# Optimization experiments

Hardware: AMD Instinct MI355X
Metric: run time of the kernel (lower is better)

Reference implementation:

```python
import jax, jax.numpy as jnp
import numpy as np
from jax import lax

VOCAB, MAX_LEN, EMB, H = 50000, 128, 300, 50
BATCH = 1024
BN_SCALE = 1.0 / np.sqrt(1.0 + 0.001)  # batch_normalization with mean=0, var=1, eps=1e-3


def setup_inputs() -> dict:
    key = jax.random.key(0)
    ks = jax.random.split(key, 10)
    return {
        "x1": jax.random.randint(ks[0], (BATCH, MAX_LEN), 0, VOCAB, dtype=jnp.int32),
        "x2": jax.random.randint(ks[1], (BATCH, MAX_LEN), 0, VOCAB, dtype=jnp.int32),
        "embedding_matrix": jax.random.normal(ks[2], (VOCAB, EMB), jnp.float32),
        "W_fw": jax.random.normal(ks[3], (EMB + H, 4 * H), jnp.float32) * 0.05,
        "b_fw": jnp.zeros((4 * H,), jnp.float32),
        "W_bw": jax.random.normal(ks[4], (EMB + H, 4 * H), jnp.float32) * 0.05,
        "b_bw": jnp.zeros((4 * H,), jnp.float32),
        "W1": jax.random.normal(ks[5], (2 * H, 25), jnp.float32) * 0.1,
        "b1": jax.random.normal(ks[6], (25,), jnp.float32) * 0.1,
        "W2": jax.random.normal(ks[7], (25, 3), jnp.float32) * 0.1,
        "b2": jax.random.normal(ks[8], (3,), jnp.float32) * 0.1,
    }


def _lstm_scan(xs, W, b):
    # xs: [T, B, E]; BasicLSTMCell: gates = [x, h] @ W + b, split i, j, f, o; forget_bias=1.0
    T, B, _ = xs.shape
    def step(carry, x):
        c, h = carry
        g = jnp.concatenate([x, h], axis=-1) @ W + b
        i, j, f, o = jnp.split(g, 4, axis=-1)
        c2 = c * jax.nn.sigmoid(f + 1.0) + jax.nn.sigmoid(i) * jnp.tanh(j)
        h2 = jnp.tanh(c2) * jax.nn.sigmoid(o)
        return (c2, h2), h2
    init = (jnp.zeros((B, H), xs.dtype), jnp.zeros((B, H), xs.dtype))
    _, hs = lax.scan(step, init, xs)
    return hs  # [T, B, H]


def reference(x1, x2, embedding_matrix, W_fw, b_fw, W_bw, b_bw, W1, b1, W2, b2):
    tokens = jnp.concatenate([x1, x2], axis=1)            # [B, 2*max_len]
    emb = embedding_matrix[tokens]                         # [B, T, E]
    xs = jnp.transpose(emb, (1, 0, 2))                     # [T, B, E]
    h_fw = _lstm_scan(xs, W_fw, b_fw)                      # [T, B, H]
    h_bw = _lstm_scan(xs[::-1], W_bw, b_bw)                # [T, B, H] (time reversed)
    # static_bidirectional_rnn reverses bw outputs, so outputs[-1] pairs
    # fw at step T-1 with bw's first step (which consumed x_{T-1}).
    feat = jnp.concatenate([h_fw[-1], h_bw[0]], axis=-1)   # [B, 2H]
    bn = feat * BN_SCALE
    h1 = jax.nn.relu(bn @ W1 + b1)                         # dropout omitted (eval mode)
    out = h1 @ W2 + b2
    return out * BN_SCALE
```

## Files before the change

### kernel.cpp

```cpp
#include <hip/hip_runtime.h>
#include <hip/hip_bf16.h>


#define VOCAB 50000
#define EMB   300
#define HID   50
#define GATES 200
#define BATCH 1024
#define TT    256
#define NPAD  208
#define KPAD  320
#define BN_SCALE 0.9995003746877732f

typedef short bf16x8 __attribute__((ext_vector_type(8)));
typedef float f32x4  __attribute__((ext_vector_type(4)));

__device__ __forceinline__ float sigm(float x) {
    return 1.0f / (1.0f + __expf(-x));
}
__device__ __forceinline__ float tanh_f(float x) {
    return 1.0f - 2.0f / (__expf(2.0f * x) + 1.0f);
}
__device__ __forceinline__ unsigned short f32_to_bf16(float x) {
    unsigned int u = __float_as_uint(x);
    u += 0x7fffu + ((u >> 16) & 1u);
    return (unsigned short)(u >> 16);
}
__device__ __forceinline__ float bf16_to_f32(unsigned short h) {
    return __uint_as_float(((unsigned int)h) << 16);
}

__global__ __launch_bounds__(256) void split_w(const float* __restrict__ Wfw,
                                               unsigned short* __restrict__ WhT,
                                               unsigned short* __restrict__ WlT) {
    const int idx = blockIdx.x * 256 + threadIdx.x;
    if (idx >= NPAD * KPAD) return;
    const int n = idx / KPAD;
    const int k = idx - n * KPAD;
    float v = (n < GATES && k < EMB) ? Wfw[k * GATES + n] : 0.0f;
    const unsigned short hb = f32_to_bf16(v);
    const unsigned short lb = f32_to_bf16(v - bf16_to_f32(hb));
    WhT[idx] = hb;
    WlT[idx] = lb;
}

__global__ __launch_bounds__(256, 1) void vocab_proj_mfma(const float* __restrict__ E,
                                                          const unsigned short* __restrict__ WhT,
                                                          const unsigned short* __restrict__ WlT,
                                                          float* __restrict__ P) {
    const int w  = threadIdx.x >> 6;
    const int l  = threadIdx.x & 63;
    const int lr = l & 15;
    const int lg = l >> 4;

    const int row0 = blockIdx.x * 128 + w * 32 + lr;
    const int row1 = row0 + 16;
    const int rc0  = (row0 < VOCAB) ? row0 : (VOCAB - 1);
    const int rc1  = (row1 < VOCAB) ? row1 : (VOCAB - 1);
    const float* Erow0 = E + (size_t)rc0 * EMB;
    const float* Erow1 = E + (size_t)rc1 * EMB;

    f32x4 acc0[13], acc1[13];
#pragma unroll
    for (int f = 0; f < 13; ++f) {
        acc0[f] = (f32x4){0.f, 0.f, 0.f, 0.f};
        acc1[f] = (f32x4){0.f, 0.f, 0.f, 0.f};
    }

    for (int ks = 0; ks < 10; ++ks) {
        const int k0 = ks * 32 + lg * 8;
        float av0[8], av1[8];
        if (ks < 9) {
            const float4 a00 = *reinterpret_cast<const float4*>(Erow0 + k0);
            const float4 a01 = *reinterpret_cast<const float4*>(Erow0 + k0 + 4);
            const float4 a10 = *reinterpret_cast<const float4*>(Erow1 + k0);
            const float4 a11 = *reinterpret_cast<const float4*>(Erow1 + k0 + 4);
            av0[0]=a00.x; av0[1]=a00.y; av0[2]=a00.z; av0[3]=a00.w;
            av0[4]=a01.x; av0[5]=a01.y; av0[6]=a01.z; av0[7]=a01.w;
            av1[0]=a10.x; av1[1]=a10.y; av1[2]=a10.z; av1[3]=a10.w;
            av1[4]=a11.x; av1[5]=a11.y; av1[6]=a11.z; av1[7]=a11.w;
        } else {
#pragma unroll
            for (int j = 0; j < 8; ++j) {
                const int kk = k0 + j;
                av0[j] = (kk < EMB) ? Erow0[kk] : 0.0f;
                av1[j] = (kk < EMB) ? Erow1[kk] : 0.0f;
            }
        }
        bf16x8 ah0, al0, ah1, al1;
#pragma unroll
        for (int j = 0; j < 8; ++j) {
            unsigned short hb = f32_to_bf16(av0[j]);
            ah0[j] = (short)hb;
            al0[j] = (short)f32_to_bf16(av0[j] - bf16_to_f32(hb));
            hb = f32_to_bf16(av1[j]);
            ah1[j] = (short)hb;
            al1[j] = (short)f32_to_bf16(av1[j] - bf16_to_f32(hb));
        }

#pragma unroll
        for (int f = 0; f < 13; ++f) {
            const int n = f * 16 + lr;
            const size_t boff = (size_t)n * KPAD + k0;
            const bf16x8 bh = *reinterpret_cast<const bf16x8*>(WhT + boff);
            const bf16x8 bl = *reinterpret_cast<const bf16x8*>(WlT + boff);
            acc0[f] = __builtin_amdgcn_mfma_f32_16x16x32_bf16(ah0, bh, acc0[f], 0, 0, 0);
            acc0[f] = __builtin_amdgcn_mfma_f32_16x16x32_bf16(al0, bh, acc0[f], 0, 0, 0);
            acc0[f] = __builtin_amdgcn_mfma_f32_16x16x32_bf16(ah0, bl, acc0[f], 0, 0, 0);
            acc1[f] = __builtin_amdgcn_mfma_f32_16x16x32_bf16(ah1, bh, acc1[f], 0, 0, 0);
            acc1[f] = __builtin_amdgcn_mfma_f32_16x16x32_bf16(al1, bh, acc1[f], 0, 0, 0);
            acc1[f] = __builtin_amdgcn_mfma_f32_16x16x32_bf16(ah1, bl, acc1[f], 0, 0, 0);
        }
    }

    const int or0 = blockIdx.x * 128 + w * 32 + lg * 4;
#pragma unroll
    for (int f = 0; f < 13; ++f) {
        const int col = f * 16 + lr;
        if (col < GATES) {
#pragma unroll
            for (int r = 0; r < 4; ++r) {
                const int oa = or0 + r;
                const int ob = oa + 16;
                if (oa < VOCAB) P[(size_t)oa * GATES + col] = acc0[f][r];
                if (ob < VOCAB) P[(size_t)ob * GATES + col] = acc1[f][r];
            }
        }
    }
}

__global__ __launch_bounds__(128, 1) void lstm_fw(const int* __restrict__ x1,
                                                  const int* __restrict__ x2,
                                                  const float* __restrict__ P,
                                                  const float* __restrict__ Wfw,
                                                  const float* __restrict__ bfw,
                                                  float* __restrict__ feat) {
    const int b = blockIdx.x;
    const int w = threadIdx.x >> 6;
    const int l = threadIdx.x & 63;
    const int u = (l < HID) ? l : (HID - 1);
    const bool act_lane = (l < HID);

    __shared__ int    stok[TT];
    __shared__ float4 ex[2][2][HID];

    stok[threadIdx.x]       = x1[b * 128 + threadIdx.x];
    stok[128 + threadIdx.x] = x2[b * 128 + threadIdx.x];

    float wi[25], wj[25], wf[25], wo[25];
#pragma unroll
    for (int k = 0; k < 25; ++k) {
        const float* rowp = Wfw + (size_t)(EMB + 25 * w + k) * GATES;
        wi[k] = rowp[u];
        wj[k] = rowp[u + 50];
        wf[k] = rowp[u + 100];
        wo[k] = rowp[u + 150];
    }
#pragma unroll
    for (int k = 0; k < 25; ++k) {
        asm volatile("" : "+v"(wi[k]), "+v"(wj[k]), "+v"(wf[k]), "+v"(wo[k]));
    }

    const float bi0 = bfw[u];
    const float bj0 = bfw[u + 50];
    const float bf0 = bfw[u + 100] + 1.0f;
    const float bo0 = bfw[u + 150];

    float c = 0.0f, h = 0.0f;
    __syncthreads();

    int tok = stok[0];
    const float* pr0 = P + (size_t)tok * GATES + u;
    float pi = pr0[0], pj = pr0[50], pf = pr0[100], po = pr0[150];
    int tokn = stok[1];

    for (int t = 0; t < TT; ++t) {
        const float cpi = pi, cpj = pj, cpf = pf, cpo = po;
        {
            const float* pn = P + (size_t)tokn * GATES + u;
            pi = pn[0]; pj = pn[50]; pf = pn[100]; po = pn[150];
        }
        tokn = stok[(t + 2 < TT) ? (t + 2) : (TT - 1)];

        float gi = 0.0f, gj = 0.0f, gf = 0.0f, go = 0.0f;
#pragma unroll
        for (int k = 0; k < 25; ++k) {
            const float hk = __uint_as_float(
                __builtin_amdgcn_readlane(__float_as_uint(h), 25 * w + k));
            gi = fmaf(wi[k], hk, gi);
            gj = fmaf(wj[k], hk, gj);
            gf = fmaf(wf[k], hk, gf);
            go = fmaf(wo[k], hk, go);
        }

        if (act_lane) ex[t & 1][w][l] = make_float4(gi, gj, gf, go);
        asm volatile("s_waitcnt lgkmcnt(0)" ::: "memory");
        __builtin_amdgcn_s_barrier();
        const float4 op = ex[t & 1][w ^ 1][u];

        const float ai = gi + op.x + cpi + bi0;
        const float aj = gj + op.y + cpj + bj0;
        const float af = gf + op.z + cpf + bf0;
        const float ao = go + op.w + cpo + bo0;

        c = c * sigm(af) + sigm(ai) * tanh_f(aj);
        h = tanh_f(c) * sigm(ao);
    }

    if (w == 0 && act_lane) feat[b * (2 * HID) + l] = h;
}

__global__ __launch_bounds__(256) void bw_mlp(const int* __restrict__ x2,
                                              const float* __restrict__ E,
                                              const float* __restrict__ Wbw,
                                              const float* __restrict__ bbw,
                                              const float* __restrict__ W1,
                                              const float* __restrict__ b1,
                                              const float* __restrict__ W2,
                                              const float* __restrict__ b2,
                                              const float* __restrict__ featfw,
                                              float* __restrict__ out) {
    const int b = blockIdx.x;
    const int t = threadIdx.x;

    __shared__ __align__(16) float sx[EMB + 4];
    __shared__ float sf[2 * HID];
    __shared__ float sg[GATES];
    __shared__ float sh1[25];

    const int tok = x2[b * 128 + 127];
    for (int e = t; e < EMB; e += 256) sx[e] = E[(size_t)tok * EMB + e];
    if (t < HID) sf[t] = featfw[b * (2 * HID) + t];
    __syncthreads();

    if (t < GATES) {
        float g0 = bbw[t], g1 = 0.0f, g2 = 0.0f, g3 = 0.0f;
        for (int e = 0; e < EMB; e += 4) {
            g0 = fmaf(sx[e + 0], Wbw[(e + 0) * GATES + t], g0);
            g1 = fmaf(sx[e + 1], Wbw[(e + 1) * GATES + t], g1);
            g2 = fmaf(sx[e + 2], Wbw[(e + 2) * GATES + t], g2);
            g3 = fmaf(sx[e + 3], Wbw[(e + 3) * GATES + t], g3);
        }
        sg[t] = (g0 + g1) + (g2 + g3);
    }
    __syncthreads();

    if (t < HID) {
        const float c2 = sigm(sg[t]) * tanh_f(sg[t + HID]);
        sf[HID + t] = tanh_f(c2) * sigm(sg[t + 3 * HID]);
    }
    __syncthreads();

    if (t < 25) {
        float a = 0.0f;
#pragma unroll 4
        for (int k = 0; k < 2 * HID; ++k)
            a = fmaf(sf[k], W1[k * 25 + t], a);
        a = fmaf(a, BN_SCALE, b1[t]);
        sh1[t] = fmaxf(a, 0.0f);
    }
    __syncthreads();

    if (t < 3) {
        float a = b2[t];
#pragma unroll
        for (int k = 0; k < 25; ++k)
            a = fmaf(sh1[k], W2[k * 3 + t], a);
        out[b * 3 + t] = a * BN_SCALE;
    }
}

extern "C" void kernel_launch(void* const* d_in, const int* in_sizes, int n_in,
                              void* d_out, int out_size, void* d_ws, size_t ws_size,
                              hipStream_t stream) {
    const int*   x1  = (const int*)d_in[0];
    const int*   x2  = (const int*)d_in[1];
    const float* E   = (const float*)d_in[2];
    const float* Wfw = (const float*)d_in[3];
    const float* bfw = (const float*)d_in[4];
    const float* Wbw = (const float*)d_in[5];
    const float* bbw = (const float*)d_in[6];
    const float* W1  = (const float*)d_in[7];
    const float* b1  = (const float*)d_in[8];
    const float* W2  = (const float*)d_in[9];
    const float* b2  = (const float*)d_in[10];
    float* out = (float*)d_out;

    float* Pm   = (float*)d_ws;
    float* feat = Pm + (size_t)VOCAB * GATES;
    unsigned short* WhT = (unsigned short*)(feat + BATCH * 2 * HID);
    unsigned short* WlT = WhT + (size_t)NPAD * KPAD;

    split_w<<<(NPAD * KPAD + 255) / 256, 256, 0, stream>>>(Wfw, WhT, WlT);
    vocab_proj_mfma<<<(VOCAB + 127) / 128, 256, 0, stream>>>(E, WhT, WlT, Pm);
    lstm_fw<<<BATCH, 128, 0, stream>>>(x1, x2, Pm, Wfw, bfw, feat);
    bw_mlp<<<BATCH, 256, 0, stream>>>(x2, E, Wbw, bbw, W1, b1, W2, b2, feat, out);
}
```

Before: 468.0 us.

## Batch 16 rows per block and compute LSTM recurrence with split-bf16 MFMA

Replaces the per-row forward LSTM kernel with one that processes 16 batch rows per block. The recurrent h@W product runs on bf16 MFMA, using hi/lo splitting of both h and W to keep near-fp32 accuracy. Gates are exchanged through LDS so activations run per (row, unit). This cuts the serial readlane/FMA chain and the redundant weight loads, but leaves only 64 blocks, adds a second barrier per step, and issues several gathered P loads per lane.

```diff
diff --git a/kernel.cpp b/kernel.cpp
--- a/kernel.cpp
+++ b/kernel.cpp
@@ -8,6 +8,7 @@
 #define GATES 200
 #define BATCH 1024
 #define TT    256
+#define RB    16
 #define NPAD  208
 #define KPAD  320
 #define BN_SCALE 0.9995003746877732f
@@ -29,6 +30,9 @@
 __device__ __forceinline__ float bf16_to_f32(unsigned short h) {
     return __uint_as_float(((unsigned int)h) << 16);
 }
+
+#define BARRIER() do { asm volatile("s_waitcnt lgkmcnt(0)" ::: "memory"); \
+                       __builtin_amdgcn_s_barrier(); } while (0)
 
 __global__ __launch_bounds__(256) void split_w(const float* __restrict__ Wfw,
                                                unsigned short* __restrict__ WhT,
@@ -129,85 +133,159 @@
     }
 }
 
-__global__ __launch_bounds__(128, 1) void lstm_fw(const int* __restrict__ x1,
-                                                  const int* __restrict__ x2,
-                                                  const float* __restrict__ P,
-                                                  const float* __restrict__ Wfw,
-                                                  const float* __restrict__ bfw,
-                                                  float* __restrict__ feat) {
-    const int b = blockIdx.x;
-    const int w = threadIdx.x >> 6;
-    const int l = threadIdx.x & 63;
-    const int u = (l < HID) ? l : (HID - 1);
-    const bool act_lane = (l < HID);
-
-    __shared__ int    stok[TT];
-    __shared__ float4 ex[2][2][HID];
-
-    stok[threadIdx.x]       = x1[b * 128 + threadIdx.x];
-    stok[128 + threadIdx.x] = x2[b * 128 + threadIdx.x];
-
-    float wi[25], wj[25], wf[25], wo[25];
-#pragma unroll
-    for (int k = 0; k < 25; ++k) {
-        const float* rowp = Wfw + (size_t)(EMB + 25 * w + k) * GATES;
-        wi[k] = rowp[u];
-        wj[k] = rowp[u + 50];
-        wf[k] = rowp[u + 100];
-        wo[k] = rowp[u + 150];
-    }
-#pragma unroll
-    for (int k = 0; k < 25; ++k) {
-        asm volatile("" : "+v"(wi[k]), "+v"(wj[k]), "+v"(wf[k]), "+v"(wo[k]));
-    }
-
+__global__ __launch_bounds__(256, 1) void lstm_fw_mfma(const int* __restrict__ x1,
+                                                       const int* __restrict__ x2,
+                                                       const float* __restrict__ P,
+                                                       const float* __restrict__ Wfw,
+                                                       const float* __restrict__ bfw,
+                                                       float* __restrict__ feat) {
+    const int blk = blockIdx.x;
+    const int tid = threadIdx.x;
+    const int w   = tid >> 6;
+    const int l   = tid & 63;
+    const int lr  = l & 15;
+    const int lg  = l >> 4;
+
+    __shared__ __align__(16) int   toks[RB][TT];
+    __shared__ __align__(16) float glds[GATES][20];
+    __shared__ __align__(16) unsigned short hhi[RB][72];
+    __shared__ __align__(16) unsigned short hlo[RB][72];
+
+    for (int i = tid; i < RB * 128; i += 256) {
+        const int r = i >> 7, p = i & 127;
+        toks[r][p]       = x1[(blk * RB + r) * 128 + p];
+        toks[r][128 + p] = x2[(blk * RB + r) * 128 + p];
+    }
+    for (int i = tid; i < RB * 72; i += 256) {
+        (&hhi[0][0])[i] = 0;
+        (&hlo[0][0])[i] = 0;
+    }
+
+    const int nfrag = (w < 3) ? 3 : 4;
+    const int fg0   = (w < 3) ? w * 3 : 9;
+
+    bf16x8 Bh[4][2], Bl[4][2];
+#pragma unroll
+    for (int q = 0; q < 4; ++q) {
+#pragma unroll
+        for (int ks = 0; ks < 2; ++ks) {
+            const int col = (fg0 + q) * 16 + lr;
+#pragma unroll
+            for (int j = 0; j < 8; ++j) {
+                const int k = ks * 32 + lg * 8 + j;
+                const float v = (q < nfrag && col < GATES && k < HID)
+                                ? Wfw[(size_t)(EMB + k) * GATES + col] : 0.0f;
+                const unsigned short hb = f32_to_bf16(v);
+                Bh[q][ks][j] = (short)hb;
+                Bl[q][ks][j] = (short)f32_to_bf16(v - bf16_to_f32(hb));
+            }
+        }
+    }
+
+    const int u  = tid % 50;
+    const int rg = tid / 50;
+    const bool act = tid < 200;
     const float bi0 = bfw[u];
     const float bj0 = bfw[u + 50];
     const float bf0 = bfw[u + 100] + 1.0f;
     const float bo0 = bfw[u + 150];
 
-    float c = 0.0f, h = 0.0f;
-    __syncthreads();
-
-    int tok = stok[0];
-    const float* pr0 = P + (size_t)tok * GATES + u;
-    float pi = pr0[0], pj = pr0[50], pf = pr0[100], po = pr0[150];
-    int tokn = stok[1];
+    float cst[4]  = {0.f, 0.f, 0.f, 0.f};
+    float harr[4] = {0.f, 0.f, 0.f, 0.f};
+
+    __syncthreads();
+
+    f32x4 pP[4];
+    {
+        int tk[4];
+#pragma unroll
+        for (int rr = 0; rr < 4; ++rr) tk[rr] = toks[lg * 4 + rr][0];
+#pragma unroll
+        for (int q = 0; q < 4; ++q) {
+            const int col = (fg0 + q) * 16 + lr;
+#pragma unroll
+            for (int rr = 0; rr < 4; ++rr)
+                pP[q][rr] = (q < nfrag && col < GATES)
+                            ? P[(size_t)tk[rr] * GATES + col] : 0.0f;
+        }
+    }
 
     for (int t = 0; t < TT; ++t) {
-        const float cpi = pi, cpj = pj, cpf = pf, cpo = po;
+        const bf16x8 Ah0 = *reinterpret_cast<const bf16x8*>(&hhi[lr][lg * 8]);
+        const bf16x8 Al0 = *reinterpret_cast<const bf16x8*>(&hlo[lr][lg * 8]);
+        const bf16x8 Ah1 = *reinterpret_cast<const bf16x8*>(&hhi[lr][32 + lg * 8]);
+        const bf16x8 Al1 = *reinterpret_cast<const bf16x8*>(&hlo[lr][32 + lg * 8]);
+
+        f32x4 acc[4];
+#pragma unroll
+        for (int q = 0; q < 4; ++q) acc[q] = pP[q];
+
         {
-            const float* pn = P + (size_t)tokn * GATES + u;
-            pi = pn[0]; pj = pn[50]; pf = pn[100]; po = pn[150];
-        }
-        tokn = stok[(t + 2 < TT) ? (t + 2) : (TT - 1)];
-
-        float gi = 0.0f, gj = 0.0f, gf = 0.0f, go = 0.0f;
-#pragma unroll
-        for (int k = 0; k < 25; ++k) {
-            const float hk = __uint_as_float(
-                __builtin_amdgcn_readlane(__float_as_uint(h), 25 * w + k));
-            gi = fmaf(wi[k], hk, gi);
-            gj = fmaf(wj[k], hk, gj);
-            gf = fmaf(wf[k], hk, gf);
-            go = fmaf(wo[k], hk, go);
-        }
-
-        if (act_lane) ex[t & 1][w][l] = make_float4(gi, gj, gf, go);
-        asm volatile("s_waitcnt lgkmcnt(0)" ::: "memory");
-        __builtin_amdgcn_s_barrier();
-        const float4 op = ex[t & 1][w ^ 1][u];
-
-        const float ai = gi + op.x + cpi + bi0;
-        const float aj = gj + op.y + cpj + bj0;
-        const float af = gf + op.z + cpf + bf0;
-        const float ao = go + op.w + cpo + bo0;
-
-        c = c * sigm(af) + sigm(ai) * tanh_f(aj);
-        h = tanh_f(c) * sigm(ao);
-    }
-
-    if (w == 0 && act_lane) feat[b * (2 * HID) + l] = h;
+            const int tn = (t + 1 < TT) ? t + 1 : TT - 1;
+            int tk[4];
+#pragma unroll
+            for (int rr = 0; rr < 4; ++rr) tk[rr] = toks[lg * 4 + rr][tn];
+#pragma unroll
+            for (int q = 0; q < 4; ++q) {
+                const int col = (fg0 + q) * 16 + lr;
+#pragma unroll
+                for (int rr = 0; rr < 4; ++rr)
+                    pP[q][rr] = (q < nfrag && col < GATES)
+                                ? P[(size_t)tk[rr] * GATES + col] : 0.0f;
+            }
+        }
+
+#pragma unroll
+        for (int q = 0; q < 4; ++q) {
+            if (q < nfrag) {
+                acc[q] = __builtin_amdgcn_mfma_f32_16x16x32_bf16(Ah0, Bh[q][0], acc[q], 0, 0, 0);
+                acc[q] = __builtin_amdgcn_mfma_f32_16x16x32_bf16(Al0, Bh[q][0], acc[q], 0, 0, 0);
+                acc[q] = __builtin_amdgcn_mfma_f32_16x16x32_bf16(Ah0, Bl[q][0], acc[q], 0, 0, 0);
+                acc[q] = __builtin_amdgcn_mfma_f32_16x16x32_bf16(Ah1, Bh[q][1], acc[q], 0, 0, 0);
+                acc[q] = __builtin_amdgcn_mfma_f32_16x16x32_bf16(Al1, Bh[q][1], acc[q], 0, 0, 0);
+                acc[q] = __builtin_amdgcn_mfma_f32_16x16x32_bf16(Ah1, Bl[q][1], acc[q], 0, 0, 0);
+            }
+        }
+
+#pragma unroll
+        for (int q = 0; q < 4; ++q) {
+            const int col = (fg0 + q) * 16 + lr;
+            if (q < nfrag && col < GATES)
+                *reinterpret_cast<f32x4*>(&glds[col][lg * 4]) = acc[q];
+        }
+
+        BARRIER();
+
+        if (act) {
+            const f32x4 gi4 = *reinterpret_cast<const f32x4*>(&glds[u][rg * 4]);
+            const f32x4 gj4 = *reinterpret_cast<const f32x4*>(&glds[u +  50][rg * 4]);
+            const f32x4 gf4 = *reinterpret_cast<const f32x4*>(&glds[u + 100][rg * 4]);
+            const f32x4 go4 = *reinterpret_cast<const f32x4*>(&glds[u + 150][rg * 4]);
+#pragma unroll
+            for (int rr = 0; rr < 4; ++rr) {
+                const float ai = gi4[rr] + bi0;
+                const float aj = gj4[rr] + bj0;
+                const float af = gf4[rr] + bf0;
+                const float ao = go4[rr] + bo0;
+                float c = cst[rr];
+                c = c * sigm(af) + sigm(ai) * tanh_f(aj);
+                cst[rr] = c;
+                const float h = tanh_f(c) * sigm(ao);
+                harr[rr] = h;
+                const unsigned short hb = f32_to_bf16(h);
+                hhi[rg * 4 + rr][u] = hb;
+                hlo[rg * 4 + rr][u] = f32_to_bf16(h - bf16_to_f32(hb));
+            }
+        }
+
+        BARRIER();
+    }
+
+    if (act) {
+#pragma unroll
+        for (int rr = 0; rr < 4; ++rr)
+            feat[(size_t)(blk * RB + rg * 4 + rr) * (2 * HID) + u] = harr[rr];
+    }
 }
 
 __global__ __launch_bounds__(256) void bw_mlp(const int* __restrict__ x2,
@@ -293,6 +371,6 @@
 
     split_w<<<(NPAD * KPAD + 255) / 256, 256, 0, stream>>>(Wfw, WhT, WlT);
     vocab_proj_mfma<<<(VOCAB + 127) / 128, 256, 0, stream>>>(E, WhT, WlT, Pm);
-    lstm_fw<<<BATCH, 128, 0, stream>>>(x1, x2, Pm, Wfw, bfw, feat);
+    lstm_fw_mfma<<<BATCH / RB, 256, 0, stream>>>(x1, x2, Pm, Wfw, bfw, feat);
     bw_mlp<<<BATCH, 256, 0, stream>>>(x2, E, Wbw, bbw, W1, b1, W2, b2, feat, out);
 }
```

Result: slower. 594.5 us (+27.0%).
